# Kernel optimization log

Measured on AMD Instinct MI355X. Metric: run time of the kernel, lower is better.

The kernel has to match this reference:

```python
import jax, jax.numpy as jnp
import numpy as np

# Complete A-ary tree of depth D, nodes stored in level order.
# Children of node i are A*i+1 .. A*i+A.
B, A, D = 512, 4, 6
N = (A**D - 1) // (A - 1)  # 1365 nodes per tree
V, E_EMB, E_ENC = 50000, 128, 128


def setup_inputs() -> dict:
    key = jax.random.key(0)
    ks = jax.random.split(key, 5)
    tokens = jax.random.randint(ks[0], (B, N), 0, V)
    emb = jax.random.normal(ks[1], (V, E_EMB), jnp.float32) * 0.02
    Wc_W = jax.random.normal(ks[2], (E_ENC, E_EMB), jnp.float32) / np.sqrt(E_EMB)
    Wc_b = jnp.zeros((E_ENC,), jnp.float32)
    Ws_W = jax.random.normal(ks[3], (E_ENC, E_ENC), jnp.float32) / np.sqrt(E_ENC)
    Ws_b = jnp.zeros((E_ENC,), jnp.float32)
    return {"tokens": tokens, "emb": emb, "Wc_W": Wc_W, "Wc_b": Wc_b,
            "Ws_W": Ws_W, "Ws_b": Ws_b, "bs": B}


def reference(tokens, emb, Wc_W, Wc_b, Ws_W, Ws_b, bs):
    # Per-node local term: W_c(embedding(token))  -> [B, N, E]
    e = emb[tokens] @ Wc_W.T + Wc_b
    level_sizes = [A ** d for d in range(D)]
    starts = np.cumsum([0] + level_sizes)  # static offsets into level order

    # Bottom-up recurrence: h(node) = e(node) + sum_children W_sum(h(child)).
    # W_sum (incl. bias) is applied per child then summed, matching the
    # per-child-slot index_copy + Linear in the original recursion.
    hs = [None] * D
    hs[D - 1] = e[:, starts[D - 1]:starts[D]]  # leaves
    for d in range(D - 2, -1, -1):
        child = hs[d + 1]                        # [B, A^(d+1), E]
        proj = child @ Ws_W.T + Ws_b             # W_sum per child
        agg = proj.reshape(bs, level_sizes[d], A, E_ENC).sum(axis=2)
        hs[d] = e[:, starts[d]:starts[d + 1]] + agg

    h_all = jnp.concatenate(hs, axis=1)          # [B, N, E]
    # node_list holds activation(h) per tree position; combine = max over nodes
    return jnp.max(jax.nn.relu(h_all), axis=1)   # [B, E]
```

## Files before the change

kernel.cpp:

```cpp
#include <hip/hip_runtime.h>
#include <hip/hip_bf16.h>

#define NTOK 1365
#define ED   128
#define STR  136
#define VROWS 50000
#define PROWS 50048

typedef __attribute__((ext_vector_type(8))) short short8;
typedef __attribute__((ext_vector_type(4))) float f32x4;

#define MFMA(a,b,c) __builtin_amdgcn_mfma_f32_16x16x32_bf16((a),(b),(c),0,0,0)

#define BAR() do {                                                   \
    __builtin_amdgcn_fence(__ATOMIC_RELEASE, "workgroup", "local");  \
    __builtin_amdgcn_s_barrier();                                    \
    __builtin_amdgcn_fence(__ATOMIC_ACQUIRE, "workgroup", "local");  \
  } while (0)

__device__ __forceinline__ ushort f2bf(float f) {
  union { float f; unsigned u; } v; v.f = f;
  unsigned r = v.u + 0x7fffu + ((v.u >> 16) & 1u);
  return (ushort)(r >> 16);
}
__device__ __forceinline__ ushort4 cvt4(float4 f) {
  ushort4 u; u.x = f2bf(f.x); u.y = f2bf(f.y); u.z = f2bf(f.z); u.w = f2bf(f.w);
  return u;
}
__device__ __forceinline__ short8 pack8(float4 a, float4 b) {
  union { ushort us[8]; short8 s8; } t;
  t.us[0]=f2bf(a.x); t.us[1]=f2bf(a.y); t.us[2]=f2bf(a.z); t.us[3]=f2bf(a.w);
  t.us[4]=f2bf(b.x); t.us[5]=f2bf(b.y); t.us[6]=f2bf(b.z); t.us[7]=f2bf(b.w);
  return t.s8;
}

__global__ __attribute__((amdgpu_flat_work_group_size(256, 256)))
void proj_kernel(const float* __restrict__ emb, const float* __restrict__ WcW,
                 const float* __restrict__ Wcb, ushort* __restrict__ P) {
  __shared__ ushort At[64 * STR];
  const int tid = threadIdx.x, w = tid >> 6, lane = tid & 63;
  const int n16 = lane & 15, quad = lane >> 4, kof = quad * 8;
  const int m0 = blockIdx.x * 64;

  #pragma unroll
  for (int i = 0; i < 8; i++) {
    const int idx = tid + i*256;
    const int r = idx >> 5, c4 = idx & 31;
    int arow = m0 + r; if (arow >= VROWS) arow = 0;
    float4 f = ((const float4*)(emb + (long)arow*ED))[c4];
    *(ushort4*)(At + r*STR + (c4 << 2)) = cvt4(f);
  }

  float bv[2];
  short8 Bp[2][4];
  #pragma unroll
  for (int j = 0; j < 2; j++) {
    const int c = w*32 + j*16 + n16;
    bv[j] = Wcb[c];
    #pragma unroll
    for (int kb = 0; kb < 4; kb++) {
      const float* pc = WcW + c*ED + kb*32 + kof;
      Bp[j][kb] = pack8(((const float4*)pc)[0], ((const float4*)pc)[1]);
    }
  }
  __syncthreads();

  #pragma unroll
  for (int i = 0; i < 4; i++) {
    f32x4 acc0 = (f32x4){0.f,0.f,0.f,0.f}, acc1 = (f32x4){0.f,0.f,0.f,0.f};
    #pragma unroll
    for (int kb = 0; kb < 4; kb++) {
      short8 a = *(const short8*)(At + (i*16 + n16)*STR + kb*32 + kof);
      acc0 = MFMA(a, Bp[0][kb], acc0);
      acc1 = MFMA(a, Bp[1][kb], acc1);
    }
    #pragma unroll
    for (int r = 0; r < 4; r++) {
      const int orow = m0 + i*16 + quad*4 + r;
      if (orow < VROWS) {
        P[(long)orow*ED + w*32 + n16]      = f2bf(acc0[r] + bv[0]);
        P[(long)orow*ED + w*32 + 16 + n16] = f2bf(acc1[r] + bv[1]);
      }
    }
  }
}

#define TKB 5472
#define SMP_BYTES (TKB + 148 * STR * 2)

__global__ __attribute__((amdgpu_flat_work_group_size(512, 512),
                          amdgpu_waves_per_eu(4, 4)))
void tree_kernel_p(
    const int* __restrict__ tokens, const ushort* __restrict__ P,
    const float* __restrict__ WsW,  const float* __restrict__ Wsb,
    float* __restrict__ out) {
  extern __shared__ char smem[];
  int*    TK  = (int*)smem;
  ushort* CS4 = (ushort*)(smem + TKB);
  ushort* CS3 = CS4 + 64*STR;
  ushort* CS2 = CS3 + 64*STR;
  ushort* CS1 = CS2 + 16*STR;
  float*  PM  = (float*)CS4;

  const int  tid = threadIdx.x;
  const int  b   = blockIdx.x;
  const int  w    = tid >> 6;
  const int  lane = tid & 63;
  const int  n16  = lane & 15;
  const int  quad = lane >> 4;
  const int  mtg  = w >> 2, ntg = w & 3;
  const int  kof  = quad * 8;

  {
    const long tokbase = (long)b * NTOK;
    for (int i = tid; i < NTOK; i += 512) TK[i] = tokens[tokbase + i];
  }

  float bsv[2];
  #pragma unroll
  for (int j = 0; j < 2; j++) bsv[j] = 4.f * Wsb[ntg*32 + j*16 + n16];

  short8 Bs[2][4];
  #pragma unroll
  for (int jt = 0; jt < 2; jt++)
    #pragma unroll
    for (int kb = 0; kb < 4; kb++) {
      const float* pc = WsW + (ntg*32 + jt*16 + n16)*ED + kb*32 + kof;
      Bs[jt][kb] = pack8(((const float4*)pc)[0], ((const float4*)pc)[1]);
    }

  short8 I2[2];
  #pragma unroll
  for (int j = 0; j < 2; j++) {
    union { ushort us[8]; short8 s8; } t;
    #pragma unroll
    for (int e = 0; e < 8; e++) t.us[e] = 0;
    if (quad == 2*j + (n16 >> 3)) t.us[n16 & 7] = 0x3F80;
    I2[j] = t.s8;
  }

  float pm[2] = {0.f, 0.f};

  short8 FA[2], FB[2];
  auto issueF = [&](short8 (&F)[2], int ofs) {
    const int co = ntg*32 + kof;
    F[0] = *(const short8*)(P + (long)TK[ofs + mtg*32      + n16]*ED + co);
    F[1] = *(const short8*)(P + (long)TK[ofs + mtg*32 + 16 + n16]*ED + co);
  };
  auto issueS = [&](short8 (&F)[2], int ofs, int M) {
    if (mtg != 0) return;
    const int ar = (M == 16) ? n16 : ((M == 4) ? (n16 & 3) : 0);
    F[0] = *(const short8*)(P + (long)TK[ofs + ar]*ED + ntg*32 + kof);
  };

  auto phase64 = [&](const short8 (&F)[2], const ushort* csrc, ushort* csdst,
                     int csrow0) {
    f32x4 acc[2][2];
    #pragma unroll
    for (int i = 0; i < 2; i++)
      #pragma unroll
      for (int j = 0; j < 2; j++) acc[i][j] = (f32x4){0.f,0.f,0.f,0.f};
    acc[0][0]=MFMA(F[0],I2[0],acc[0][0]); acc[0][1]=MFMA(F[0],I2[1],acc[0][1]);
    acc[1][0]=MFMA(F[1],I2[0],acc[1][0]); acc[1][1]=MFMA(F[1],I2[1],acc[1][1]);
    if (csrc) {
      #pragma unroll
      for (int kb = 0; kb < 4; kb++) {
        const int ko = kb*32 + kof;
        short8 c0 = *(const short8*)(csrc + (mtg*32      + n16)*STR + ko);
        short8 c1 = *(const short8*)(csrc + (mtg*32 + 16 + n16)*STR + ko);
        acc[0][0]=MFMA(c0,Bs[0][kb],acc[0][0]); acc[0][1]=MFMA(c0,Bs[1][kb],acc[0][1]);
        acc[1][0]=MFMA(c1,Bs[0][kb],acc[1][0]); acc[1][1]=MFMA(c1,Bs[1][kb],acc[1][1]);
      }
    }
    #pragma unroll
    for (int i = 0; i < 2; i++) {
      const int p = mtg*8 + i*4 + quad;
      #pragma unroll
      for (int j = 0; j < 2; j++) {
        const float bb = csrc ? bsv[j] : 0.f;
        f32x4 A = acc[i][j];
        float h0=A[0]+bb, h1=A[1]+bb, h2=A[2]+bb, h3=A[3]+bb;
        pm[j] = fmaxf(pm[j], fmaxf(fmaxf(h0,h1), fmaxf(h2,h3)));
        csdst[(csrow0 + p)*STR + ntg*32 + j*16 + n16] =
            f2bf(A[0]+A[1]+A[2]+A[3] + 4.f*bb);
      }
    }
  };

  auto smallphase = [&](short8 a, const ushort* csrc, int M, ushort* csdst) {
    if (mtg != 0) return;
    const int ar = (M == 16) ? n16 : ((M == 4) ? (n16 & 3) : 0);
    f32x4 acc[2];
    acc[0] = (f32x4){0.f,0.f,0.f,0.f}; acc[1] = (f32x4){0.f,0.f,0.f,0.f};
    acc[0] = MFMA(a, I2[0], acc[0]); acc[1] = MFMA(a, I2[1], acc[1]);
    #pragma unroll
    for (int kb = 0; kb < 4; kb++) {
      const int ko = kb*32 + kof;
      short8 c2 = *(const short8*)(csrc + ar*STR + ko);
      acc[0] = MFMA(c2, Bs[0][kb], acc[0]); acc[1] = MFMA(c2, Bs[1][kb], acc[1]);
    }
    #pragma unroll
    for (int j = 0; j < 2; j++) {
      const float bb = bsv[j];
      f32x4 A = acc[j];
      const int c = ntg*32 + j*16 + n16;
      if (M == 16) {
        float h0=A[0]+bb, h1=A[1]+bb, h2=A[2]+bb, h3=A[3]+bb;
        pm[j] = fmaxf(pm[j], fmaxf(fmaxf(h0,h1), fmaxf(h2,h3)));
        csdst[quad*STR + c] = f2bf(A[0]+A[1]+A[2]+A[3] + 4.f*bb);
      } else if (M == 4) {
        if (quad == 0) {
          float h0=A[0]+bb, h1=A[1]+bb, h2=A[2]+bb, h3=A[3]+bb;
          pm[j] = fmaxf(pm[j], fmaxf(fmaxf(h0,h1), fmaxf(h2,h3)));
          csdst[c] = f2bf(A[0]+A[1]+A[2]+A[3] + 4.f*bb);
        }
      } else {
        if (quad == 0) pm[j] = fmaxf(pm[j], A[0] + bb);
      }
    }
  };

  __syncthreads();
  issueF(FA, 341);
   issueF(FB, 405);  phase64(FA, nullptr, CS4,  0);
   issueF(FA, 469);  phase64(FB, nullptr, CS4, 16);
   issueF(FB, 533);  phase64(FA, nullptr, CS4, 32);
   issueF(FA, 85);   phase64(FB, nullptr, CS4, 48); BAR();
   issueF(FB, 597);   phase64(FA, CS4,     CS3,  0); BAR();
   issueF(FA, 661);  phase64(FB, nullptr, CS4,  0);
   issueF(FB, 725);  phase64(FA, nullptr, CS4, 16);
   issueF(FA, 789);  phase64(FB, nullptr, CS4, 32);
   issueF(FB, 149);  phase64(FA, nullptr, CS4, 48); BAR();
   issueF(FA, 853);   phase64(FB, CS4,     CS3, 16); BAR();
   issueF(FB, 917);  phase64(FA, nullptr, CS4,  0);
   issueF(FA, 981);  phase64(FB, nullptr, CS4, 16);
   issueF(FB, 1045); phase64(FA, nullptr, CS4, 32);
   issueF(FA, 213);  phase64(FB, nullptr, CS4, 48); BAR();
   issueF(FB, 1109);  phase64(FA, CS4,     CS3, 32); BAR();
   issueF(FA, 1173); phase64(FB, nullptr, CS4,  0);
   issueF(FB, 1237); phase64(FA, nullptr, CS4, 16);
   issueF(FA, 1301); phase64(FB, nullptr, CS4, 32);
   issueF(FB, 277);  phase64(FA, nullptr, CS4, 48); BAR();
   issueF(FA, 21);    phase64(FB, CS4,     CS3, 48); BAR();
  issueS(FB, 5, 16);                   phase64(FA, CS3,     CS2,  0);
  for (int i = tid; i < 1024; i += 512) PM[i] = 0.f;
  BAR();
   issueS(FA, 1, 4);   smallphase(FB[0], CS2, 16, CS1); BAR();
   issueS(FB, 0, 1);   smallphase(FA[0], CS1, 4,  CS2); BAR();
                       smallphase(FB[0], CS2, 1,  nullptr);

  #pragma unroll
  for (int j = 0; j < 2; j++) {
    float v = pm[j];
    v = fmaxf(v, __shfl_xor(v, 16, 64));
    v = fmaxf(v, __shfl_xor(v, 32, 64));
    if (quad == 0) PM[w*128 + ntg*32 + j*16 + n16] = v;
  }
  __syncthreads();
  if (tid < 128) {
    float m = 0.f;
    #pragma unroll
    for (int r = 0; r < 8; r++) m = fmaxf(m, PM[r*128 + tid]);
    out[(long)b*ED + tid] = m;
  }
}

#define SM_BYTES (4096 + 404 * STR * 2)

__global__ __attribute__((amdgpu_flat_work_group_size(512, 512),
                          amdgpu_waves_per_eu(2, 8)))
void tree_kernel(
    const int* __restrict__ tokens, const float* __restrict__ emb,
    const float* __restrict__ WcW,  const float* __restrict__ Wcb,
    const float* __restrict__ WsW,  const float* __restrict__ Wsb,
    float* __restrict__ out) {
  extern __shared__ char smem[];
  float*  PM  = (float*)smem;
  ushort* WsL = (ushort*)(PM + 1024);
  ushort* Xe0 = WsL + 128*STR;
  ushort* Xe1 = Xe0 + 64*STR;
  ushort* CS4 = Xe1 + 64*STR;
  ushort* CS3 = CS4 + 64*STR;
  ushort* CS2 = CS3 + 64*STR;
  ushort* CS1 = CS2 + 16*STR;

  const int  tid = threadIdx.x;
  const int  b   = blockIdx.x;
  const long tokbase = (long)b * NTOK;
  const int  w    = tid >> 6;
  const int  lane = tid & 63;
  const int  n16  = lane & 15;
  const int  quad = lane >> 4;
  const int  mtg  = w >> 2, ntg = w & 3;
  const int  kof  = quad * 8;

  float bcv[2], bsv[2];
  #pragma unroll
  for (int j = 0; j < 2; j++) {
    const int c = ntg*32 + j*16 + n16;
    bcv[j] = Wcb[c]; bsv[j] = 4.f * Wsb[c];
  }

  short8 Bc[2][4];
  #pragma unroll
  for (int jt = 0; jt < 2; jt++)
    #pragma unroll
    for (int kb = 0; kb < 4; kb++) {
      const float* pc = WcW + (ntg*32 + jt*16 + n16)*ED + kb*32 + kof;
      Bc[jt][kb] = pack8(((const float4*)pc)[0], ((const float4*)pc)[1]);
    }

  #pragma unroll
  for (int i = 0; i < 8; i++) {
    const int idx = tid + i*512;
    float4 f = ((const float4*)WsW)[idx];
    *(ushort4*)(WsL + (idx >> 5)*STR + ((idx & 31) << 2)) = cvt4(f);
  }

  for (int i = tid; i < 1024; i += 512) PM[i] = 0.f;
  float pm[2] = {0.f, 0.f};

  float4 RA[4], RB[4];
  auto issue64 = [&](float4 (&R)[4], int ofs) {
    const int r = tid >> 3, p = tid & 7;
    const float4* src = (const float4*)(emb + (long)tokens[tokbase + ofs + r]*ED) + (p << 2);
    R[0] = src[0]; R[1] = src[1]; R[2] = src[2]; R[3] = src[3];
  };
  auto store64 = [&](const float4 (&R)[4], ushort* Xe) {
    const int r = tid >> 3, p = tid & 7;
    short8* d = (short8*)(Xe + r*STR + (p << 4));
    d[0] = pack8(R[0], R[1]); d[1] = pack8(R[2], R[3]);
  };
  auto issueN = [&](float4 (&R)[4], int ofs, int nrows) {
    const int r = tid >> 5, p = tid & 31;
    if (r < nrows) R[0] = ((const float4*)(emb + (long)tokens[tokbase + ofs + r]*ED))[p];
  };
  auto storeN = [&](const float4 (&R)[4], ushort* Xe, int nrows) {
    const int r = tid >> 5, p = tid & 31;
    if (r < nrows) *(ushort4*)(Xe + r*STR + (p << 2)) = cvt4(R[0]);
  };

  auto phase64 = [&](const ushort* Xe, const ushort* csrc, ushort* csdst, int csrow0) {
    f32x4 acc[2][2];
    #pragma unroll
    for (int i = 0; i < 2; i++)
      #pragma unroll
      for (int j = 0; j < 2; j++) acc[i][j] = (f32x4){0.f,0.f,0.f,0.f};
    #pragma unroll
    for (int kb = 0; kb < 4; kb++) {
      const int ko = kb*32 + kof;
      short8 a0 = *(const short8*)(Xe + (mtg*32      + n16)*STR + ko);
      short8 a1 = *(const short8*)(Xe + (mtg*32 + 16 + n16)*STR + ko);
      acc[0][0]=MFMA(a0,Bc[0][kb],acc[0][0]); acc[0][1]=MFMA(a0,Bc[1][kb],acc[0][1]);
      acc[1][0]=MFMA(a1,Bc[0][kb],acc[1][0]); acc[1][1]=MFMA(a1,Bc[1][kb],acc[1][1]);
      if (csrc) {
        short8 c0 = *(const short8*)(csrc + (mtg*32      + n16)*STR + ko);
        short8 c1 = *(const short8*)(csrc + (mtg*32 + 16 + n16)*STR + ko);
        short8 s0 = *(const short8*)(WsL  + (ntg*32      + n16)*STR + ko);
        short8 s1 = *(const short8*)(WsL  + (ntg*32 + 16 + n16)*STR + ko);
        acc[0][0]=MFMA(c0,s0,acc[0][0]); acc[0][1]=MFMA(c0,s1,acc[0][1]);
        acc[1][0]=MFMA(c1,s0,acc[1][0]); acc[1][1]=MFMA(c1,s1,acc[1][1]);
      }
    }
    #pragma unroll
    for (int i = 0; i < 2; i++) {
      const int p = mtg*8 + i*4 + quad;
      #pragma unroll
      for (int j = 0; j < 2; j++) {
        const float bb = csrc ? (bcv[j] + bsv[j]) : bcv[j];
        f32x4 A = acc[i][j];
        float h0=A[0]+bb, h1=A[1]+bb, h2=A[2]+bb, h3=A[3]+bb;
        pm[j] = fmaxf(pm[j], fmaxf(fmaxf(h0,h1), fmaxf(h2,h3)));
        csdst[(csrow0 + p)*STR + ntg*32 + j*16 + n16] =
            f2bf(A[0]+A[1]+A[2]+A[3] + 4.f*bb);
      }
    }
  };

  auto smallphase = [&](const ushort* Xe, const ushort* csrc, int M, ushort* csdst) {
    if (mtg != 0) return;
    const int ar = (M == 16) ? n16 : ((M == 4) ? (n16 & 3) : 0);
    f32x4 acc[2];
    acc[0] = (f32x4){0.f,0.f,0.f,0.f}; acc[1] = (f32x4){0.f,0.f,0.f,0.f};
    #pragma unroll
    for (int kb = 0; kb < 4; kb++) {
      const int ko = kb*32 + kof;
      short8 a  = *(const short8*)(Xe   + ar*STR + ko);
      short8 c2 = *(const short8*)(csrc + ar*STR + ko);
      short8 s0 = *(const short8*)(WsL + (ntg*32      + n16)*STR + ko);
      short8 s1 = *(const short8*)(WsL + (ntg*32 + 16 + n16)*STR + ko);
      acc[0] = MFMA(a,  Bc[0][kb], acc[0]); acc[1] = MFMA(a,  Bc[1][kb], acc[1]);
      acc[0] = MFMA(c2, s0, acc[0]);        acc[1] = MFMA(c2, s1, acc[1]);
    }
    #pragma unroll
    for (int j = 0; j < 2; j++) {
      const float bb = bcv[j] + bsv[j];
      f32x4 A = acc[j];
      const int c = ntg*32 + j*16 + n16;
      if (M == 16) {
        float h0=A[0]+bb, h1=A[1]+bb, h2=A[2]+bb, h3=A[3]+bb;
        pm[j] = fmaxf(pm[j], fmaxf(fmaxf(h0,h1), fmaxf(h2,h3)));
        csdst[quad*STR + c] = f2bf(A[0]+A[1]+A[2]+A[3] + 4.f*bb);
      } else if (M == 4) {
        if (quad == 0) {
          float h0=A[0]+bb, h1=A[1]+bb, h2=A[2]+bb, h3=A[3]+bb;
          pm[j] = fmaxf(pm[j], fmaxf(fmaxf(h0,h1), fmaxf(h2,h3)));
          csdst[c] = f2bf(A[0]+A[1]+A[2]+A[3] + 4.f*bb);
        }
      } else {
        if (quad == 0) pm[j] = fmaxf(pm[j], A[0] + bb);
      }
    }
  };

  issue64(RA, 341);
  issue64(RB, 341 + 64);
  store64(RA, Xe0);
  __syncthreads();
  issue64(RA, 341+128);     phase64(Xe0, nullptr, CS4,  0); store64(RB, Xe1); __syncthreads();
  issue64(RB, 341+192);     phase64(Xe1, nullptr, CS4, 16); store64(RA, Xe0); __syncthreads();
  issue64(RA, 85);          phase64(Xe0, nullptr, CS4, 32); store64(RB, Xe1); __syncthreads();
  issue64(RB, 341+256);     phase64(Xe1, nullptr, CS4, 48); store64(RA, Xe0); __syncthreads();
  issue64(RA, 341+256+64);  phase64(Xe0, CS4,     CS3,  0); store64(RB, Xe1); __syncthreads();
  issue64(RB, 341+256+128); phase64(Xe1, nullptr, CS4,  0); store64(RA, Xe0); __syncthreads();
  issue64(RA, 341+256+192); phase64(Xe0, nullptr, CS4, 16); store64(RB, Xe1); __syncthreads();
  issue64(RB, 85+64);       phase64(Xe1, nullptr, CS4, 32); store64(RA, Xe0); __syncthreads();
  issue64(RA, 341+512);     phase64(Xe0, nullptr, CS4, 48); store64(RB, Xe1); __syncthreads();
  issue64(RB, 341+512+64);  phase64(Xe1, CS4,     CS3, 16); store64(RA, Xe0); __syncthreads();
  issue64(RA, 341+512+128); phase64(Xe0, nullptr, CS4,  0); store64(RB, Xe1); __syncthreads();
  issue64(RB, 341+512+192); phase64(Xe1, nullptr, CS4, 16); store64(RA, Xe0); __syncthreads();
  issue64(RA, 85+128);      phase64(Xe0, nullptr, CS4, 32); store64(RB, Xe1); __syncthreads();
  issue64(RB, 341+768);     phase64(Xe1, nullptr, CS4, 48); store64(RA, Xe0); __syncthreads();
  issue64(RA, 341+768+64);  phase64(Xe0, CS4,     CS3, 32); store64(RB, Xe1); __syncthreads();
  issue64(RB, 341+768+128); phase64(Xe1, nullptr, CS4,  0); store64(RA, Xe0); __syncthreads();
  issue64(RA, 341+768+192); phase64(Xe0, nullptr, CS4, 16); store64(RB, Xe1); __syncthreads();
  issue64(RB, 85+192);      phase64(Xe1, nullptr, CS4, 32); store64(RA, Xe0); __syncthreads();
  issue64(RA, 21);          phase64(Xe0, nullptr, CS4, 48); store64(RB, Xe1); __syncthreads();
  issueN(RB, 5, 16);        phase64(Xe1, CS4,     CS3, 48); store64(RA, Xe0); __syncthreads();
  issueN(RA, 1, 4);         phase64(Xe0, CS3,     CS2,  0); storeN(RB, Xe1, 16); __syncthreads();
  issueN(RB, 0, 1);         smallphase(Xe1, CS2, 16, CS1);  storeN(RA, Xe0, 4);  __syncthreads();
                            smallphase(Xe0, CS1, 4,  CS2);  storeN(RB, Xe1, 1);  __syncthreads();
                            smallphase(Xe1, CS2, 1,  nullptr);

  #pragma unroll
  for (int j = 0; j < 2; j++) {
    float v = pm[j];
    v = fmaxf(v, __shfl_xor(v, 16, 64));
    v = fmaxf(v, __shfl_xor(v, 32, 64));
    if (quad == 0) PM[w*128 + ntg*32 + j*16 + n16] = v;
  }
  __syncthreads();
  if (tid < 128) {
    float m = 0.f;
    #pragma unroll
    for (int r = 0; r < 8; r++) m = fmaxf(m, PM[r*128 + tid]);
    out[(long)b*ED + tid] = m;
  }
}

extern "C" void kernel_launch(void* const* d_in, const int* in_sizes, int n_in,
                              void* d_out, int out_size, void* d_ws, size_t ws_size,
                              hipStream_t stream) {
  const int*   tokens = (const int*)d_in[0];
  const float* emb    = (const float*)d_in[1];
  const float* WcW    = (const float*)d_in[2];
  const float* Wcb    = (const float*)d_in[3];
  const float* WsW    = (const float*)d_in[4];
  const float* Wsb    = (const float*)d_in[5];
  float* out = (float*)d_out;

  const size_t needP = (size_t)PROWS * ED * sizeof(ushort);
  if (d_ws != nullptr && ws_size >= needP) {
    ushort* P = (ushort*)d_ws;
    proj_kernel<<<(VROWS + 63) / 64, 256, 0, stream>>>(emb, WcW, Wcb, P);
    hipFuncSetAttribute(reinterpret_cast<const void*>(tree_kernel_p),
                        hipFuncAttributeMaxDynamicSharedMemorySize, SMP_BYTES);
    tree_kernel_p<<<512, 512, SMP_BYTES, stream>>>(tokens, P, WsW, Wsb, out);
  } else {
    hipFuncSetAttribute(reinterpret_cast<const void*>(tree_kernel),
                        hipFuncAttributeMaxDynamicSharedMemorySize, SM_BYTES);
    tree_kernel<<<512, 512, SM_BYTES, stream>>>(tokens, emb, WcW, Wcb, WsW, Wsb, out);
  }
}
```

Baseline: 127.9 us.

## Split per-tree kernel into quarter-subtree blocks plus tail kernel

The single per-tree kernel (512 blocks) becomes two kernels. The first runs 2048 blocks, each handling one quarter of the bottom two levels of one tree, and writes level-3 child sums and partial maxima to workspace. A tail kernel per tree then finishes the upper levels and combines the partial maxima. This raises parallelism beyond one block per tree, at the cost of an extra launch, global round-trips for intermediates, and a larger workspace requirement. If the workspace is too small, the code silently falls back to the slow path.

```diff
diff --git a/kernel.cpp b/kernel.cpp
--- a/kernel.cpp
+++ b/kernel.cpp
@@ -6,6 +6,13 @@
 #define STR  136
 #define VROWS 50000
 #define PROWS 50048
+
+#define P_BYTES  ((size_t)PROWS * ED * 2)
+#define G3_OFF   P_BYTES
+#define G3_BYTES ((size_t)512 * 64 * ED * 2)
+#define GPM_OFF  (G3_OFF + G3_BYTES)
+#define GPM_BYTES ((size_t)512 * 4 * ED * 4)
+#define WS_NEED  (GPM_OFF + GPM_BYTES)
 
 typedef __attribute__((ext_vector_type(8))) short short8;
 typedef __attribute__((ext_vector_type(4))) float f32x4;
@@ -85,35 +92,29 @@
   }
 }
 
-#define TKB 5472
-#define SMP_BYTES (TKB + 148 * STR * 2)
-
 __global__ __attribute__((amdgpu_flat_work_group_size(512, 512),
                           amdgpu_waves_per_eu(4, 4)))
-void tree_kernel_p(
-    const int* __restrict__ tokens, const ushort* __restrict__ P,
-    const float* __restrict__ WsW,  const float* __restrict__ Wsb,
-    float* __restrict__ out) {
-  extern __shared__ char smem[];
-  int*    TK  = (int*)smem;
-  ushort* CS4 = (ushort*)(smem + TKB);
-  ushort* CS3 = CS4 + 64*STR;
-  ushort* CS2 = CS3 + 64*STR;
-  ushort* CS1 = CS2 + 16*STR;
-  float*  PM  = (float*)CS4;
-
-  const int  tid = threadIdx.x;
-  const int  b   = blockIdx.x;
-  const int  w    = tid >> 6;
-  const int  lane = tid & 63;
-  const int  n16  = lane & 15;
-  const int  quad = lane >> 4;
-  const int  mtg  = w >> 2, ntg = w & 3;
-  const int  kof  = quad * 8;
-
-  {
+void tree_q(const int* __restrict__ tokens, const ushort* __restrict__ P,
+            const float* __restrict__ WsW,  const float* __restrict__ Wsb,
+            ushort* __restrict__ G3, float* __restrict__ GPM) {
+  __shared__ int    TK[320];
+  __shared__ ushort CS4[64 * STR];
+  __shared__ ushort CS3q[16 * STR];
+  __shared__ float  PM[1024];
+
+  const int tid = threadIdx.x;
+  const int bq  = blockIdx.x, b = bq >> 2, q = bq & 3;
+  const int w    = tid >> 6;
+  const int lane = tid & 63;
+  const int n16  = lane & 15;
+  const int quad = lane >> 4;
+  const int mtg  = w >> 2, ntg = w & 3;
+  const int kof  = quad * 8;
+
+  if (tid < 320) {
     const long tokbase = (long)b * NTOK;
-    for (int i = tid; i < NTOK; i += 512) TK[i] = tokens[tokbase + i];
+    TK[tid] = (tid < 256) ? tokens[tokbase + 341 + q*256 + tid]
+                          : tokens[tokbase + 85 + q*64 + (tid - 256)];
   }
 
   float bsv[2];
@@ -146,11 +147,6 @@
     const int co = ntg*32 + kof;
     F[0] = *(const short8*)(P + (long)TK[ofs + mtg*32      + n16]*ED + co);
     F[1] = *(const short8*)(P + (long)TK[ofs + mtg*32 + 16 + n16]*ED + co);
-  };
-  auto issueS = [&](short8 (&F)[2], int ofs, int M) {
-    if (mtg != 0) return;
-    const int ar = (M == 16) ? n16 : ((M == 4) ? (n16 & 3) : 0);
-    F[0] = *(const short8*)(P + (long)TK[ofs + ar]*ED + ntg*32 + kof);
   };
 
   auto phase64 = [&](const short8 (&F)[2], const ushort* csrc, ushort* csdst,
@@ -178,6 +174,132 @@
       #pragma unroll
       for (int j = 0; j < 2; j++) {
         const float bb = csrc ? bsv[j] : 0.f;
+        f32x4 A = acc[i][j];
+        float h0=A[0]+bb, h1=A[1]+bb, h2=A[2]+bb, h3=A[3]+bb;
+        pm[j] = fmaxf(pm[j], fmaxf(fmaxf(h0,h1), fmaxf(h2,h3)));
+        csdst[(csrow0 + p)*STR + ntg*32 + j*16 + n16] =
+            f2bf(A[0]+A[1]+A[2]+A[3] + 4.f*bb);
+      }
+    }
+  };
+
+  __syncthreads();
+  issueF(FA, 0);
+   issueF(FB, 64);  phase64(FA, nullptr, CS4,  0);
+   issueF(FA, 128); phase64(FB, nullptr, CS4, 16);
+   issueF(FB, 192); phase64(FA, nullptr, CS4, 32);
+   issueF(FA, 256); phase64(FB, nullptr, CS4, 48); BAR();
+                    phase64(FA, CS4,     CS3q, 0); BAR();
+
+  if (tid < 256) {
+    const int r = tid >> 4, p = tid & 15;
+    *(short8*)(G3 + ((long)(b*64 + q*16 + r))*ED + p*8) =
+        *(const short8*)(CS3q + r*STR + p*8);
+  }
+
+  #pragma unroll
+  for (int j = 0; j < 2; j++) {
+    float v = pm[j];
+    v = fmaxf(v, __shfl_xor(v, 16, 64));
+    v = fmaxf(v, __shfl_xor(v, 32, 64));
+    if (quad == 0) PM[w*128 + ntg*32 + j*16 + n16] = v;
+  }
+  __syncthreads();
+  if (tid < 128) {
+    const int c = tid, w0 = c >> 5;
+    float m = fmaxf(PM[w0*128 + c], PM[(w0+4)*128 + c]);
+    GPM[((long)b*4 + q)*ED + c] = m;
+  }
+}
+
+__global__ __attribute__((amdgpu_flat_work_group_size(512, 512),
+                          amdgpu_waves_per_eu(4, 4)))
+void tree_tail(const int* __restrict__ tokens, const ushort* __restrict__ P,
+               const float* __restrict__ WsW,  const float* __restrict__ Wsb,
+               const ushort* __restrict__ G3, const float* __restrict__ GPM,
+               float* __restrict__ out) {
+  __shared__ int    TK[96];
+  __shared__ ushort CS3[64 * STR];
+  __shared__ ushort CS2[16 * STR];
+  __shared__ ushort CS1[4 * STR];
+  __shared__ float  PM[1024];
+
+  const int tid = threadIdx.x;
+  const int b   = blockIdx.x;
+  const int w    = tid >> 6;
+  const int lane = tid & 63;
+  const int n16  = lane & 15;
+  const int quad = lane >> 4;
+  const int mtg  = w >> 2, ntg = w & 3;
+  const int kof  = quad * 8;
+
+  if (tid < 85) TK[tid] = tokens[(long)b*NTOK + tid];
+  for (int i = tid; i < 1024; i += 512) {
+    const int r = i >> 4, p = i & 15;
+    *(short8*)(CS3 + r*STR + p*8) =
+        *(const short8*)(G3 + ((long)(b*64 + r))*ED + p*8);
+  }
+
+  float bsv[2];
+  #pragma unroll
+  for (int j = 0; j < 2; j++) bsv[j] = 4.f * Wsb[ntg*32 + j*16 + n16];
+
+  short8 Bs[2][4];
+  #pragma unroll
+  for (int jt = 0; jt < 2; jt++)
+    #pragma unroll
+    for (int kb = 0; kb < 4; kb++) {
+      const float* pc = WsW + (ntg*32 + jt*16 + n16)*ED + kb*32 + kof;
+      Bs[jt][kb] = pack8(((const float4*)pc)[0], ((const float4*)pc)[1]);
+    }
+
+  short8 I2[2];
+  #pragma unroll
+  for (int j = 0; j < 2; j++) {
+    union { ushort us[8]; short8 s8; } t;
+    #pragma unroll
+    for (int e = 0; e < 8; e++) t.us[e] = 0;
+    if (quad == 2*j + (n16 >> 3)) t.us[n16 & 7] = 0x3F80;
+    I2[j] = t.s8;
+  }
+
+  float pm[2] = {0.f, 0.f};
+
+  short8 FA[2], FB[2];
+  auto issueF = [&](short8 (&F)[2], int ofs) {
+    const int co = ntg*32 + kof;
+    F[0] = *(const short8*)(P + (long)TK[ofs + mtg*32      + n16]*ED + co);
+    F[1] = *(const short8*)(P + (long)TK[ofs + mtg*32 + 16 + n16]*ED + co);
+  };
+  auto issueS = [&](short8 (&F)[2], int ofs, int M) {
+    if (mtg != 0) return;
+    const int ar = (M == 16) ? n16 : ((M == 4) ? (n16 & 3) : 0);
+    F[0] = *(const short8*)(P + (long)TK[ofs + ar]*ED + ntg*32 + kof);
+  };
+
+  auto phase64 = [&](const short8 (&F)[2], const ushort* csrc, ushort* csdst,
+                     int csrow0) {
+    f32x4 acc[2][2];
+    #pragma unroll
+    for (int i = 0; i < 2; i++)
+      #pragma unroll
+      for (int j = 0; j < 2; j++) acc[i][j] = (f32x4){0.f,0.f,0.f,0.f};
+    acc[0][0]=MFMA(F[0],I2[0],acc[0][0]); acc[0][1]=MFMA(F[0],I2[1],acc[0][1]);
+    acc[1][0]=MFMA(F[1],I2[0],acc[1][0]); acc[1][1]=MFMA(F[1],I2[1],acc[1][1]);
+    #pragma unroll
+    for (int kb = 0; kb < 4; kb++) {
+      const int ko = kb*32 + kof;
+      short8 c0 = *(const short8*)(csrc + (mtg*32      + n16)*STR + ko);
+      short8 c1 = *(const short8*)(csrc + (mtg*32 + 16 + n16)*STR + ko);
+      acc[0][0]=MFMA(c0,Bs[0][kb],acc[0][0]); acc[0][1]=MFMA(c0,Bs[1][kb],acc[0][1]);
+      acc[1][0]=MFMA(c1,Bs[0][kb],acc[1][0]); acc[1][1]=MFMA(c1,Bs[1][kb],acc[1][1]);
+    }
+    #pragma unroll
+    for (int i = 0; i < 2; i++) {
+      const int p = mtg*8 + i*4 + quad;
+      #pragma unroll
+      for (int j = 0; j < 2; j++) {
+        const float bb = bsv[j];
         f32x4 A = acc[i][j];
         float h0=A[0]+bb, h1=A[1]+bb, h2=A[2]+bb, h3=A[3]+bb;
         pm[j] = fmaxf(pm[j], fmaxf(fmaxf(h0,h1), fmaxf(h2,h3)));
@@ -221,30 +343,8 @@
   };
 
   __syncthreads();
-  issueF(FA, 341);
-   issueF(FB, 405);  phase64(FA, nullptr, CS4,  0);
-   issueF(FA, 469);  phase64(FB, nullptr, CS4, 16);
-   issueF(FB, 533);  phase64(FA, nullptr, CS4, 32);
-   issueF(FA, 85);   phase64(FB, nullptr, CS4, 48); BAR();
-   issueF(FB, 597);   phase64(FA, CS4,     CS3,  0); BAR();
-   issueF(FA, 661);  phase64(FB, nullptr, CS4,  0);
-   issueF(FB, 725);  phase64(FA, nullptr, CS4, 16);
-   issueF(FA, 789);  phase64(FB, nullptr, CS4, 32);
-   issueF(FB, 149);  phase64(FA, nullptr, CS4, 48); BAR();
-   issueF(FA, 853);   phase64(FB, CS4,     CS3, 16); BAR();
-   issueF(FB, 917);  phase64(FA, nullptr, CS4,  0);
-   issueF(FA, 981);  phase64(FB, nullptr, CS4, 16);
-   issueF(FB, 1045); phase64(FA, nullptr, CS4, 32);
-   issueF(FA, 213);  phase64(FB, nullptr, CS4, 48); BAR();
-   issueF(FB, 1109);  phase64(FA, CS4,     CS3, 32); BAR();
-   issueF(FA, 1173); phase64(FB, nullptr, CS4,  0);
-   issueF(FB, 1237); phase64(FA, nullptr, CS4, 16);
-   issueF(FA, 1301); phase64(FB, nullptr, CS4, 32);
-   issueF(FB, 277);  phase64(FA, nullptr, CS4, 48); BAR();
-   issueF(FA, 21);    phase64(FB, CS4,     CS3, 48); BAR();
-  issueS(FB, 5, 16);                   phase64(FA, CS3,     CS2,  0);
-  for (int i = tid; i < 1024; i += 512) PM[i] = 0.f;
-  BAR();
+  issueF(FA, 21);
+   issueS(FB, 5, 16);  phase64(FA, CS3, CS2, 0);        BAR();
    issueS(FA, 1, 4);   smallphase(FB[0], CS2, 16, CS1); BAR();
    issueS(FB, 0, 1);   smallphase(FA[0], CS1, 4,  CS2); BAR();
                        smallphase(FB[0], CS2, 1,  nullptr);
@@ -258,10 +358,11 @@
   }
   __syncthreads();
   if (tid < 128) {
-    float m = 0.f;
-    #pragma unroll
-    for (int r = 0; r < 8; r++) m = fmaxf(m, PM[r*128 + tid]);
-    out[(long)b*ED + tid] = m;
+    const int c = tid, w0 = c >> 5;
+    float m = fmaxf(PM[w0*128 + c], PM[(w0+4)*128 + c]);
+    #pragma unroll
+    for (int q = 0; q < 4; q++) m = fmaxf(m, GPM[((long)b*4 + q)*ED + c]);
+    out[(long)b*ED + c] = m;
   }
 }
 
@@ -469,13 +570,13 @@
   const float* Wsb    = (const float*)d_in[5];
   float* out = (float*)d_out;
 
-  const size_t needP = (size_t)PROWS * ED * sizeof(ushort);
-  if (d_ws != nullptr && ws_size >= needP) {
-    ushort* P = (ushort*)d_ws;
+  if (d_ws != nullptr && ws_size >= WS_NEED) {
+    ushort* P   = (ushort*)d_ws;
+    ushort* G3  = (ushort*)((char*)d_ws + G3_OFF);
+    float*  GPM = (float*)((char*)d_ws + GPM_OFF);
     proj_kernel<<<(VROWS + 63) / 64, 256, 0, stream>>>(emb, WcW, Wcb, P);
-    hipFuncSetAttribute(reinterpret_cast<const void*>(tree_kernel_p),
-                        hipFuncAttributeMaxDynamicSharedMemorySize, SMP_BYTES);
-    tree_kernel_p<<<512, 512, SMP_BYTES, stream>>>(tokens, P, WsW, Wsb, out);
+    tree_q<<<2048, 512, 0, stream>>>(tokens, P, WsW, Wsb, G3, GPM);
+    tree_tail<<<512, 512, 0, stream>>>(tokens, P, WsW, Wsb, G3, GPM, out);
   } else {
     hipFuncSetAttribute(reinterpret_cast<const void*>(tree_kernel),
                         hipFuncAttributeMaxDynamicSharedMemorySize, SM_BYTES);
```

Measured after the change: 183.0 us. 1.43x slower.
